# Kernel tuning notes

Hardware: AMD Instinct MI355X
Metric: run time of the kernel (lower is better)

Reference implementation:

```python
import jax, jax.numpy as jnp
import numpy as np

NUM_HEADS = 16


def rotate_half(x):
    half = x.shape[-1] // 2
    return jnp.concatenate((-x[..., half:], x[..., :half]), axis=-1)


def rope_tables(seq_len, head_dim, dtype=jnp.float32):
    inv_freq = 1.0 / (10000.0 ** (jnp.arange(0, head_dim, 2, dtype=jnp.float32) / head_dim))
    t = jnp.arange(seq_len, dtype=jnp.float32)
    freqs = jnp.outer(t, inv_freq)                 # [S, hd/2]
    emb = jnp.concatenate((freqs, freqs), axis=-1)  # [S, hd]
    return jnp.cos(emb).astype(dtype), jnp.sin(emb).astype(dtype)


def setup_inputs() -> dict:
    key = jax.random.key(0)
    k1, k2, k3 = jax.random.split(key, 3)
    B, S, D = 2, 2048, 1024
    x = jax.random.normal(k1, (B, S, D), dtype=jnp.float32)
    # causal lower-triangular mask, broadcast over batch/heads
    mask = jnp.tril(jnp.ones((S, S), dtype=bool))[None, None, :, :]
    w_qkv = jax.random.normal(k2, (3 * D, D), dtype=jnp.float32) * (D ** -0.5)
    w_out = jax.random.normal(k3, (D, D), dtype=jnp.float32) * (D ** -0.5)
    return {"x": x, "mask": mask, "w_qkv": w_qkv, "w_out": w_out}


def reference(x, mask, w_qkv, w_out):
    B, S, D = x.shape
    H = NUM_HEADS
    hd = D // H
    scale = hd ** -0.5

    qkv = jnp.einsum('bsd,ed->bse', x, w_qkv)          # [B, S, 3D]
    q, k, v = jnp.split(qkv, 3, axis=-1)

    def split(t):
        return t.reshape(B, S, H, hd).transpose(0, 2, 1, 3)  # [B, H, S, hd]

    q, k, v = split(q), split(k), split(v)

    cos, sin = rope_tables(S, hd, x.dtype)             # [S, hd]
    cos = cos[None, None]
    sin = sin[None, None]
    q = q * cos + rotate_half(q) * sin
    k = k * cos + rotate_half(k) * sin

    attn = jnp.einsum('bhqd,bhkd->bhqk', q, k) * scale  # [B, H, S, S]
    attn = jnp.where(mask, attn, jnp.float32(-jnp.inf).astype(attn.dtype))
    attn = jax.nn.softmax(attn, axis=-1)
    out = jnp.einsum('bhqk,bhkd->bhqd', attn, v)        # [B, H, S, hd]
    out = out.transpose(0, 2, 1, 3).reshape(B, S, D)
    return jnp.einsum('bsd,ed->bse', out, w_out)
```

## Files before the change

kernel.cpp:

```cpp
#include <hip/hip_runtime.h>
#include <hip/hip_bf16.h>

typedef __attribute__((ext_vector_type(8))) __bf16 bf16x8;
typedef __attribute__((ext_vector_type(4))) __bf16 bf16x4;
typedef __attribute__((ext_vector_type(2))) __bf16 bf16x2;
typedef __attribute__((ext_vector_type(4))) float f32x4;
typedef __attribute__((ext_vector_type(16))) float f32x16;

#define SEQ 2048
#define NH 16
#define HD 64
#define DMODEL 1024
#define BATCH 2
#define MTOT 4096
#define NSLOT 72

#if __has_builtin(__builtin_amdgcn_exp2f)
#define EXP2(x) __builtin_amdgcn_exp2f(x)
#else
#define EXP2(x) exp2f(x)
#endif
#define MFMA32(a, b, c) __builtin_amdgcn_mfma_f32_32x32x16_bf16(a, b, c, 0, 0, 0)

__device__ __forceinline__ void gl_lds16(const void* g, void* l) {
    __builtin_amdgcn_global_load_lds(
        (const __attribute__((address_space(1))) void*)(uintptr_t)g,
        (__attribute__((address_space(3))) void*)(uintptr_t)l,
        16, 0, 0);
}

__device__ __forceinline__ unsigned pk2(float x, float y) {
    union { bf16x2 h; unsigned u; } c;
    c.h = bf16x2{ (__bf16)x, (__bf16)y };
    return c.u;
}

#define TILE_SYNC(N) do {                                           \
    asm volatile("s_waitcnt vmcnt(" #N ")" ::: "memory");           \
    __builtin_amdgcn_s_barrier();                                   \
    __builtin_amdgcn_sched_barrier(0);                              \
} while (0)

__constant__ int4 FITEM[80] = {
    {31,0,16,68},{31,16,32,69},{31,32,48,70},{31,48,64,71},
    {23,0,16,37},{23,16,32,38},{23,32,48,39},
    {15,0,16,14},{15,16,32,15},
    {30,15,31,65},{30,46,62,67},
    {22,30,46,36},
    {7,0,16,-1},
    {29,0,15,60},{29,15,30,61},{29,30,45,62},{29,45,60,63},
    {30,0,15,64},{30,31,46,66},
    {22,0,15,34},{22,15,30,35},
    {21,14,29,32},{21,29,44,33},
    {28,14,29,57},{28,43,58,59},
    {14,0,15,12},{14,15,30,13},
    {27,0,14,52},{27,14,28,53},{27,28,42,54},{27,42,56,55},
    {28,0,14,56},{28,29,43,58},
    {20,0,14,28},{20,14,28,29},{20,28,42,30},
    {21,0,14,31},
    {26,13,27,49},{26,40,54,51},
    {19,26,40,27},
    {13,0,14,10},{13,14,28,11},
    {6,0,14,-1},
    {25,0,13,44},{25,13,26,45},{25,26,39,46},{25,39,52,47},
    {26,0,13,48},{26,27,40,50},
    {24,12,25,41},{24,37,50,43},
    {19,0,13,25},{19,13,26,26},
    {18,12,25,23},{18,25,38,24},
    {12,0,13,8},{12,13,26,9},
    {24,0,12,40},{24,25,37,42},
    {17,0,12,19},{17,12,24,20},{17,24,36,21},
    {18,0,12,22},
    {16,22,34,18},
    {11,0,12,6},{11,12,24,7},
    {5,0,12,-1},
    {16,0,11,16},{16,11,22,17},
    {10,0,11,4},{10,11,22,5},
    {9,0,10,2},{9,10,20,3},
    {4,0,10,-1},
    {8,0,9,0},{8,9,18,1},
    {3,0,8,-1},{2,0,6,-1},{1,0,4,-1},{0,0,2,-1}
};

__global__ __launch_bounds__(256) void cast3(const float4* __restrict__ x,
                                             const float4* __restrict__ wq,
                                             const float4* __restrict__ wo,
                                             __bf16* __restrict__ xb,
                                             __bf16* __restrict__ wqb,
                                             __bf16* __restrict__ wob) {
    const int NX  = 1024 * 1024;
    const int NWQ = 768 * 1024;
    const int NTOT = NX + NWQ + 256 * 1024;
    int i = blockIdx.x * 256 + threadIdx.x;
    if (i >= NTOT) return;
    float4 v; __bf16* dst; int j;
    if (i < NX)            { j = i;            v = x[j];  dst = xb;  }
    else if (i < NX + NWQ) { j = i - NX;       v = wq[j]; dst = wqb; }
    else                   { j = i - NX - NWQ; v = wo[j]; dst = wob; }
    bf16x4 o = { (__bf16)v.x, (__bf16)v.y, (__bf16)v.z, (__bf16)v.w };
    *(bf16x4*)(dst + (size_t)j * 4) = o;
}

__global__ __launch_bounds__(512, 2) void gemm_qkv(const __bf16* __restrict__ A,
                                                   const __bf16* __restrict__ Bt,
                                                   __bf16* __restrict__ Qp,
                                                   char* __restrict__ K2,
                                                   char* __restrict__ V2) {
    const int K = 1024;
    __shared__ __align__(16) char lds[3 * 49152];
    const int tid = threadIdx.x, lane = tid & 63, wave = tid >> 6;
    const int lrow = lane & 15, quad = lane >> 4;
    const int bx = blockIdx.x, by = blockIdx.y;
    const int m0 = by * 256, n0 = bx * 128;
    const int wm = wave >> 1, wn = wave & 1;

    const __bf16* ap[4]; int aof[4];
    const __bf16* bp[2]; int bof[2];
#pragma unroll
    for (int i = 0; i < 4; ++i) {
        int r0 = i * 64 + wave * 8;
        int row = r0 + (lane >> 3);
        int cg = (lane & 7) ^ (row & 7);
        ap[i] = A + (size_t)(m0 + row) * K + cg * 8;
        aof[i] = r0 * 128;
    }
#pragma unroll
    for (int i = 0; i < 2; ++i) {
        int r0 = i * 64 + wave * 8;
        int row = r0 + (lane >> 3);
        int cg = (lane & 7) ^ (row & 7);
        bp[i] = Bt + (size_t)(n0 + row) * K + cg * 8;
        bof[i] = 32768 + r0 * 128;
    }
    int arow[4], brow[4];
#pragma unroll
    for (int i = 0; i < 4; ++i) {
        arow[i] = wm * 64 + i * 16 + lrow;
        brow[i] = wn * 64 + i * 16 + lrow;
    }

    f32x4 z = {0.f, 0.f, 0.f, 0.f};
    f32x4 acc[4][4];
#pragma unroll
    for (int i = 0; i < 4; ++i)
#pragma unroll
        for (int j = 0; j < 4; ++j) acc[i][j] = z;

    auto STAGE = [&](char* base, int k0) {
#pragma unroll
        for (int i = 0; i < 4; ++i) gl_lds16(ap[i] + k0, base + aof[i]);
#pragma unroll
        for (int i = 0; i < 2; ++i) gl_lds16(bp[i] + k0, base + bof[i]);
    };
    auto COMPUTE = [&](const char* base) {
        const char* bb = base + 32768;
#pragma unroll
        for (int ks = 0; ks < 2; ++ks) {
            bf16x8 af[4], bfr[4];
#pragma unroll
            for (int i = 0; i < 4; ++i)
                af[i] = *(const bf16x8*)(base + arow[i] * 128 +
                                         (((ks * 4 + quad) ^ (arow[i] & 7)) << 4));
#pragma unroll
            for (int i = 0; i < 4; ++i)
                bfr[i] = *(const bf16x8*)(bb + brow[i] * 128 +
                                          (((ks * 4 + quad) ^ (brow[i] & 7)) << 4));
            __builtin_amdgcn_s_setprio(1);
#pragma unroll
            for (int i = 0; i < 4; ++i)
#pragma unroll
                for (int j = 0; j < 4; ++j)
                    acc[i][j] = __builtin_amdgcn_mfma_f32_16x16x32_bf16(
                        af[i], bfr[j], acc[i][j], 0, 0, 0);
            __builtin_amdgcn_s_setprio(0);
        }
    };

    STAGE(lds, 0);
    STAGE(lds + 49152, 64);
    TILE_SYNC(6);
    for (int t = 0; t < 14; ++t) {
        STAGE(lds + ((t + 2) % 3) * 49152, (t + 2) * 64);
        COMPUTE(lds + (t % 3) * 49152);
        TILE_SYNC(6);
    }
    COMPUTE(lds + 2 * 49152);
    TILE_SYNC(0);
    COMPUTE(lds);

    const int nt = bx;
    const int sec = nt >> 3;
    const int b = m0 >> 11;
    const int s0b = m0 & (SEQ - 1);
    const int h = (nt & 7) * 2 + wn;
    const int bh = b * NH + h;

    if (sec < 2) {
        const float scale = sec ? 1.0f : 0.18033688011112042f;
        char* Kb = K2 + (size_t)bh * 262144;
        float invf0 = 0.15915494309189535f *
                      exp2f(-(float)lrow * 0.4152410118609203f);
        float invf1 = invf0 * 0.01f;
#pragma unroll
        for (int i = 0; i < 4; ++i) {
            int srow0 = s0b + wm * 64 + i * 16 + quad * 4;
#pragma unroll
            for (int j = 0; j < 2; ++j) {
                float invf = j ? invf1 : invf0;
                int hdlo = j * 16 + lrow;
#pragma unroll
                for (int r = 0; r < 4; ++r) {
                    int s = srow0 + r;
                    float rev = (float)s * invf;
                    float fr = rev - floorf(rev);
                    float sn = __builtin_amdgcn_sinf(fr);
                    float cs = __builtin_amdgcn_cosf(fr);
                    float lo = acc[i][j][r], hi = acc[i][j + 2][r];
                    float olo = (lo * cs - hi * sn) * scale;
                    float ohi = (hi * cs + lo * sn) * scale;
                    if (sec == 0) {
                        size_t base = ((size_t)bh * SEQ + s) * HD + hdlo;
                        Qp[base] = (__bf16)olo;
                        Qp[base + 32] = (__bf16)ohi;
                    } else {
                        char* kt = Kb + (s >> 5) * 4096 + (s & 31) * 16 +
                                   ((lrow >> 3) & 1) * 512 + (lrow & 7) * 2;
                        *(__bf16*)(kt + j * 1024) = (__bf16)olo;
                        *(__bf16*)(kt + (j + 2) * 1024) = (__bf16)ohi;
                    }
                }
            }
        }
    } else {
        char* Vb = V2 + (size_t)bh * 262144;
#pragma unroll
        for (int i = 0; i < 4; ++i) {
            int srow0 = s0b + wm * 64 + i * 16 + quad * 4;
            int kb = srow0 >> 4, ko = srow0 & 15;
            int slot0 = ((ko >> 2) & 1) * 8 + (ko >> 3) * 4;
#pragma unroll
            for (int j = 0; j < 4; ++j) {
                int ch = j * 16 + lrow;
                bf16x4 wv = { (__bf16)acc[i][j][0], (__bf16)acc[i][j][1],
                              (__bf16)acc[i][j][2], (__bf16)acc[i][j][3] };
                *(bf16x4*)(Vb + kb * 2048 + ch * 32 + slot0 * 2) = wv;
            }
        }
    }
}

__global__ __launch_bounds__(256) void gemm_bt(const __bf16* __restrict__ A,
                                               const __bf16* __restrict__ Bt,
                                               float* __restrict__ Cf,
                                               int M, int N, int K) {
    __shared__ __bf16 sA[2][128 * 64];
    __shared__ __bf16 sB[2][128 * 64];
    const int tid = threadIdx.x, lane = tid & 63, wave = tid >> 6;
    const int lrow = lane & 15, quad = lane >> 4;

    int lin = blockIdx.y * 8 + blockIdx.x;
    lin = (lin & 7) * 32 + (lin >> 3);
    const int bx = lin & 7, by = lin >> 3;
    const int m0 = by * 128, n0 = bx * 128;
    const int wm = wave >> 1, wn = wave & 1;

    const __bf16* ap[4]; const __bf16* bp[4]; int ldso[4];
#pragma unroll
    for (int i = 0; i < 4; ++i) {
        int r0 = i * 32 + wave * 8;
        int row = r0 + (lane >> 3);
        int cg = (lane & 7) ^ (row & 7);
        ap[i] = A + (size_t)(m0 + row) * K + cg * 8;
        bp[i] = Bt + (size_t)(n0 + row) * K + cg * 8;
        ldso[i] = r0 * 128;
    }
    int arow[4], brow[4];
#pragma unroll
    for (int i = 0; i < 4; ++i) {
        arow[i] = wm * 64 + i * 16 + lrow;
        brow[i] = wn * 64 + i * 16 + lrow;
    }

    f32x4 z = {0.f, 0.f, 0.f, 0.f};
    f32x4 acc[4][4];
#pragma unroll
    for (int i = 0; i < 4; ++i)
#pragma unroll
        for (int j = 0; j < 4; ++j) acc[i][j] = z;

    char* sA0 = (char*)sA[0]; char* sA1 = (char*)sA[1];
    char* sB0 = (char*)sB[0]; char* sB1 = (char*)sB[1];

    auto STAGE = [&](char* dA, char* dB, int k0) {
#pragma unroll
        for (int i = 0; i < 4; ++i) gl_lds16(ap[i] + k0, dA + ldso[i]);
#pragma unroll
        for (int i = 0; i < 4; ++i) gl_lds16(bp[i] + k0, dB + ldso[i]);
    };
    auto COMPUTE = [&](const char* sAb, const char* sBb) {
#pragma unroll
        for (int ks = 0; ks < 2; ++ks) {
            bf16x8 af[4], bfr[4];
#pragma unroll
            for (int i = 0; i < 4; ++i)
                af[i] = *(const bf16x8*)(sAb + arow[i] * 128 +
                                         (((ks * 4 + quad) ^ (arow[i] & 7)) << 4));
#pragma unroll
            for (int i = 0; i < 4; ++i)
                bfr[i] = *(const bf16x8*)(sBb + brow[i] * 128 +
                                          (((ks * 4 + quad) ^ (brow[i] & 7)) << 4));
#pragma unroll
            for (int i = 0; i < 4; ++i)
#pragma unroll
                for (int j = 0; j < 4; ++j)
                    acc[i][j] = __builtin_amdgcn_mfma_f32_16x16x32_bf16(
                        af[i], bfr[j], acc[i][j], 0, 0, 0);
        }
    };

    STAGE(sA0, sB0, 0);
    __syncthreads();
    for (int k0 = 0; k0 < K; k0 += 128) {
        if (k0 + 64 < K) STAGE(sA1, sB1, k0 + 64);
        COMPUTE(sA0, sB0);
        __syncthreads();
        if (k0 + 128 < K) STAGE(sA0, sB0, k0 + 128);
        COMPUTE(sA1, sB1);
        __syncthreads();
    }
#pragma unroll
    for (int i = 0; i < 4; ++i)
#pragma unroll
        for (int j = 0; j < 4; ++j)
#pragma unroll
            for (int r = 0; r < 4; ++r) {
                int row = m0 + wm * 64 + i * 16 + quad * 4 + r;
                int col = n0 + wn * 64 + j * 16 + lrow;
                Cf[(size_t)row * N + col] = acc[i][j][r];
            }
}

__global__ __launch_bounds__(64) void flash_attn(const __bf16* __restrict__ Qp,
                                                 const char* __restrict__ K2,
                                                 const char* __restrict__ V2,
                                                 __bf16* __restrict__ Aout,
                                                 __bf16* __restrict__ Opart,
                                                 float* __restrict__ Lpart) {
    const int lane = threadIdx.x;
    const int ql = lane & 31, half = lane >> 5;
    const int lin = blockIdx.x;
    const int xcd = lin & 7;
    const int j = lin >> 3;
    const int item = j % 80;
    const int bgroup = j / 80;
    const int bh = bgroup * 8 + xcd;
    const int4 it = FITEM[item];
    const int s = it.x, t0 = it.y, t1 = it.z, slot = it.w;
    const int b = bh >> 4, hh = bh & 15;

    const __bf16* qb = Qp + ((size_t)bh * SEQ + s * 64 + ql) * HD + half * 8;
    bf16x8 qf0[4], qf1[4];
#pragma unroll
    for (int kc = 0; kc < 4; ++kc) {
        qf0[kc] = *(const bf16x8*)(qb + kc * 16);
        qf1[kc] = *(const bf16x8*)(qb + 32 * HD + kc * 16);
    }
    const char* Kb = K2 + (size_t)bh * 262144 + half * 512 + ql * 16;
    const char* Vb = V2 + (size_t)bh * 262144 + ql * 32 + half * 16;

    f32x16 zz = {0.f};
    f32x16 oA0 = zz, oA1 = zz, oB0 = zz, oB1 = zz;
    float lA = 0.f, lB = 0.f;
    const int dA = 2 * s, dB = 2 * s + 1;
    const int thr = ql - 4 * half;

    auto STEP = [&](int t, const bf16x8* kf, bf16x8* kn) {
        bf16x8 vf[2][2];
#pragma unroll
        for (int lo = 0; lo < 2; ++lo) {
            const char* vp = Vb + (t * 2 + lo) * 2048;
            vf[lo][0] = *(const bf16x8*)(vp);
            vf[lo][1] = *(const bf16x8*)(vp + 1024);
        }
        if (t + 1 < t1) {
            const char* kt = Kb + (t + 1) * 4096;
#pragma unroll
            for (int kc = 0; kc < 4; ++kc)
                kn[kc] = *(const bf16x8*)(kt + kc * 1024);
        }
        const bool do0 = (t != dB);
        f32x16 st0 = zz, st1 = zz;
        if (do0) {
#pragma unroll
            for (int kc = 0; kc < 4; ++kc)
                st0 = MFMA32(kf[kc], qf0[kc], st0);
        }
#pragma unroll
        for (int kc = 0; kc < 4; ++kc)
            st1 = MFMA32(kf[kc], qf1[kc], st1);

        if (do0) {
#pragma unroll
            for (int i = 0; i < 16; ++i) st0[i] = EXP2(st0[i]);
            if (t == dA) {
#pragma unroll
                for (int g = 0; g < 4; ++g)
#pragma unroll
                    for (int tt = 0; tt < 4; ++tt)
                        if (8 * g + tt > thr) st0[g * 4 + tt] = 0.f;
            }
#pragma unroll
            for (int i = 0; i < 16; ++i) lA += st0[i];
        }
#pragma unroll
        for (int i = 0; i < 16; ++i) st1[i] = EXP2(st1[i]);
        if (t == dB) {
#pragma unroll
            for (int g = 0; g < 4; ++g)
#pragma unroll
                for (int tt = 0; tt < 4; ++tt)
                    if (8 * g + tt > thr) st1[g * 4 + tt] = 0.f;
        }
#pragma unroll
        for (int i = 0; i < 16; ++i) lB += st1[i];

#pragma unroll
        for (int lo = 0; lo < 2; ++lo) {
            if (do0) {
                union { unsigned u[4]; bf16x8 v; } p0;
#pragma unroll
                for (int d = 0; d < 4; ++d)
                    p0.u[d] = pk2(st0[lo * 8 + 2 * d], st0[lo * 8 + 2 * d + 1]);
                oA0 = MFMA32(vf[lo][0], p0.v, oA0);
                oA1 = MFMA32(vf[lo][1], p0.v, oA1);
            }
            union { unsigned u[4]; bf16x8 v; } p1;
#pragma unroll
            for (int d = 0; d < 4; ++d)
                p1.u[d] = pk2(st1[lo * 8 + 2 * d], st1[lo * 8 + 2 * d + 1]);
            oB0 = MFMA32(vf[lo][0], p1.v, oB0);
            oB1 = MFMA32(vf[lo][1], p1.v, oB1);
        }
    };

    bf16x8 kA[4], kB[4];
    {
        const char* kt = Kb + t0 * 4096;
#pragma unroll
        for (int kc = 0; kc < 4; ++kc)
            kA[kc] = *(const bf16x8*)(kt + kc * 1024);
    }
    int t = t0;
    while (true) {
        STEP(t, kA, kB);
        if (++t >= t1) break;
        STEP(t, kB, kA);
        if (++t >= t1) break;
    }

    lA += __shfl_xor(lA, 32, 64);
    lB += __shfl_xor(lB, 32, 64);

    if (slot < 0) {
        float iA = 1.0f / lA, iB = 1.0f / lB;
        __bf16* oa = Aout + ((size_t)b * SEQ + s * 64 + ql) * DMODEL + hh * HD;
        __bf16* ob = oa + (size_t)32 * DMODEL;
#pragma unroll
        for (int g = 0; g < 4; ++g) {
            bf16x4 wA0 = { (__bf16)(oA0[g*4+0]*iA), (__bf16)(oA0[g*4+1]*iA),
                           (__bf16)(oA0[g*4+2]*iA), (__bf16)(oA0[g*4+3]*iA) };
            bf16x4 wA1 = { (__bf16)(oA1[g*4+0]*iA), (__bf16)(oA1[g*4+1]*iA),
                           (__bf16)(oA1[g*4+2]*iA), (__bf16)(oA1[g*4+3]*iA) };
            bf16x4 wB0 = { (__bf16)(oB0[g*4+0]*iB), (__bf16)(oB0[g*4+1]*iB),
                           (__bf16)(oB0[g*4+2]*iB), (__bf16)(oB0[g*4+3]*iB) };
            bf16x4 wB1 = { (__bf16)(oB1[g*4+0]*iB), (__bf16)(oB1[g*4+1]*iB),
                           (__bf16)(oB1[g*4+2]*iB), (__bf16)(oB1[g*4+3]*iB) };
            *(bf16x4*)(oa + 8 * g + 4 * half) = wA0;
            *(bf16x4*)(oa + 32 + 8 * g + 4 * half) = wA1;
            *(bf16x4*)(ob + 8 * g + 4 * half) = wB0;
            *(bf16x4*)(ob + 32 + 8 * g + 4 * half) = wB1;
        }
    } else {
        __bf16* oa = Opart + ((size_t)(bh * NSLOT + slot) << 12) + ql * 64;
        __bf16* ob = oa + 32 * 64;
#pragma unroll
        for (int g = 0; g < 4; ++g) {
            bf16x4 wA0 = { (__bf16)oA0[g*4+0], (__bf16)oA0[g*4+1],
                           (__bf16)oA0[g*4+2], (__bf16)oA0[g*4+3] };
            bf16x4 wA1 = { (__bf16)oA1[g*4+0], (__bf16)oA1[g*4+1],
                           (__bf16)oA1[g*4+2], (__bf16)oA1[g*4+3] };
            bf16x4 wB0 = { (__bf16)oB0[g*4+0], (__bf16)oB0[g*4+1],
                           (__bf16)oB0[g*4+2], (__bf16)oB0[g*4+3] };
            bf16x4 wB1 = { (__bf16)oB1[g*4+0], (__bf16)oB1[g*4+1],
                           (__bf16)oB1[g*4+2], (__bf16)oB1[g*4+3] };
            *(bf16x4*)(oa + 8 * g + 4 * half) = wA0;
            *(bf16x4*)(oa + 32 + 8 * g + 4 * half) = wA1;
            *(bf16x4*)(ob + 8 * g + 4 * half) = wB0;
            *(bf16x4*)(ob + 32 + 8 * g + 4 * half) = wB1;
        }
        if (!half) {
            Lpart[(bh * NSLOT + slot) * 64 + ql] = lA;
            Lpart[(bh * NSLOT + slot) * 64 + 32 + ql] = lB;
        }
    }
}

__global__ __launch_bounds__(256) void combine(const __bf16* __restrict__ Opart,
                                               const float* __restrict__ Lpart,
                                               __bf16* __restrict__ Aout) {
    const int bh = blockIdx.x;
    const int s = 8 + blockIdx.y;
    const int C = (s < 16) ? 2 : ((s < 24) ? 3 : 4);
    const int base = (s < 16) ? (s - 8) * 2
                   : (s < 24) ? 16 + (s - 16) * 3
                              : 40 + (s - 24) * 4;
    const int t = threadIdx.x;
    const int r = t >> 2, cg = (t & 3) * 16;
    float acc[16];
#pragma unroll
    for (int i = 0; i < 16; ++i) acc[i] = 0.f;
    float l = 0.f;
    for (int ci = 0; ci < C; ++ci) {
        int ch = bh * NSLOT + base + ci;
        l += Lpart[ch * 64 + r];
        const __bf16* p = Opart + ((size_t)ch << 12) + r * 64 + cg;
#pragma unroll
        for (int k = 0; k < 2; ++k) {
            bf16x8 v = ((const bf16x8*)p)[k];
#pragma unroll
            for (int j = 0; j < 8; ++j) acc[k * 8 + j] += (float)v[j];
        }
    }
    float invl = 1.0f / l;
    const int b = bh >> 4, hh = bh & 15;
    __bf16* dst = Aout + ((size_t)(b * SEQ + s * 64 + r)) * DMODEL +
                  hh * 64 + cg;
#pragma unroll
    for (int k = 0; k < 2; ++k) {
        bf16x8 w;
#pragma unroll
        for (int j = 0; j < 8; ++j) w[j] = (__bf16)(acc[k * 8 + j] * invl);
        ((bf16x8*)dst)[k] = w;
    }
}

extern "C" void kernel_launch(void* const* d_in, const int* in_sizes, int n_in,
                              void* d_out, int out_size, void* d_ws, size_t ws_size,
                              hipStream_t stream) {
    (void)in_sizes; (void)n_in; (void)out_size; (void)ws_size;
    const float* x  = (const float*)d_in[0];
    const float* wq = (const float*)d_in[2];
    const float* wo = (const float*)d_in[3];
    float* out = (float*)d_out;

    char* w = (char*)d_ws;
    __bf16* xb   = (__bf16*)(w);
    __bf16* wqb  = (__bf16*)(w + (8ull << 20));
    __bf16* wob  = (__bf16*)(w + (14ull << 20));
    __bf16* Opart= (__bf16*)(w + (16ull << 20));
    float*  Lpart= (float*) (w + (35ull << 20));
    __bf16* Qb   = (__bf16*)(w + (40ull << 20));
    char*   K2   = (char*)  (w + (48ull << 20));
    char*   V2   = (char*)  (w + (56ull << 20));
    __bf16* aob  = xb;

    cast3<<<8192, 256, 0, stream>>>((const float4*)x, (const float4*)wq,
                                    (const float4*)wo, xb, wqb, wob);
    gemm_qkv<<<dim3(24, 16), 512, 0, stream>>>(xb, wqb, Qb, K2, V2);
    flash_attn<<<2560, 64, 0, stream>>>(Qb, K2, V2, aob, Opart, Lpart);
    combine<<<dim3(32, 24), 256, 0, stream>>>(Opart, Lpart, aob);
    gemm_bt<<<dim3(8, 32), 256, 0, stream>>>(aob, wob, out, MTOT, 1024, 1024);
}
```

Before: 184.6 us.

## Prefetch V tiles one step ahead and raise wave priority around MFMA blocks

V fragments for the next key tile are now loaded together with the next K fragments into double-buffered registers, so their global-load latency overlaps the current step's compute instead of stalling the PV MFMAs. The MFMA sections are also wrapped in s_setprio to favour waves issuing matrix work. This costs extra VGPRs for the second V buffer, which may lower occupancy.

```diff
diff --git a/kernel.cpp b/kernel.cpp
--- a/kernel.cpp
+++ b/kernel.cpp
@@ -374,15 +374,14 @@
     const int dA = 2 * s, dB = 2 * s + 1;
     const int thr = ql - 4 * half;
 
-    auto STEP = [&](int t, const bf16x8* kf, bf16x8* kn) {
-        bf16x8 vf[2][2];
-#pragma unroll
-        for (int lo = 0; lo < 2; ++lo) {
-            const char* vp = Vb + (t * 2 + lo) * 2048;
-            vf[lo][0] = *(const bf16x8*)(vp);
-            vf[lo][1] = *(const bf16x8*)(vp + 1024);
-        }
+    auto STEP = [&](int t, const bf16x8* kf, bf16x8* kn,
+                    const bf16x8 (*vf)[2], bf16x8 (*vn)[2]) {
         if (t + 1 < t1) {
+            const char* vp = Vb + ((t + 1) * 2) * 2048;
+            vn[0][0] = *(const bf16x8*)(vp);
+            vn[0][1] = *(const bf16x8*)(vp + 1024);
+            vn[1][0] = *(const bf16x8*)(vp + 2048);
+            vn[1][1] = *(const bf16x8*)(vp + 3072);
             const char* kt = Kb + (t + 1) * 4096;
 #pragma unroll
             for (int kc = 0; kc < 4; ++kc)
@@ -390,6 +389,7 @@
         }
         const bool do0 = (t != dB);
         f32x16 st0 = zz, st1 = zz;
+        __builtin_amdgcn_s_setprio(1);
         if (do0) {
 #pragma unroll
             for (int kc = 0; kc < 4; ++kc)
@@ -398,6 +398,7 @@
 #pragma unroll
         for (int kc = 0; kc < 4; ++kc)
             st1 = MFMA32(kf[kc], qf1[kc], st1);
+        __builtin_amdgcn_s_setprio(0);
 
         if (do0) {
 #pragma unroll
@@ -424,6 +425,7 @@
 #pragma unroll
         for (int i = 0; i < 16; ++i) lB += st1[i];
 
+        __builtin_amdgcn_s_setprio(1);
 #pragma unroll
         for (int lo = 0; lo < 2; ++lo) {
             if (do0) {
@@ -441,20 +443,26 @@
             oB0 = MFMA32(vf[lo][0], p1.v, oB0);
             oB1 = MFMA32(vf[lo][1], p1.v, oB1);
         }
+        __builtin_amdgcn_s_setprio(0);
     };
 
-    bf16x8 kA[4], kB[4];
+    bf16x8 kA[4], kB[4], vA[2][2], vB[2][2];
     {
         const char* kt = Kb + t0 * 4096;
 #pragma unroll
         for (int kc = 0; kc < 4; ++kc)
             kA[kc] = *(const bf16x8*)(kt + kc * 1024);
+        const char* vp = Vb + (t0 * 2) * 2048;
+        vA[0][0] = *(const bf16x8*)(vp);
+        vA[0][1] = *(const bf16x8*)(vp + 1024);
+        vA[1][0] = *(const bf16x8*)(vp + 2048);
+        vA[1][1] = *(const bf16x8*)(vp + 3072);
     }
     int t = t0;
     while (true) {
-        STEP(t, kA, kB);
+        STEP(t, kA, kB, vA, vB);
         if (++t >= t1) break;
-        STEP(t, kB, kA);
+        STEP(t, kB, kA, vB, vA);
         if (++t >= t1) break;
     }
 
```

After: 188.5 us. 2.1% more time.

## Group four attention work items per block and share K/V tiles through LDS

Applied to the files above, without the earlier changes.

Work items are reordered into groups of four with overlapping key ranges. Each 256-thread block now runs one group, one item per wave, and cooperatively stages each K/V tile into a triple-buffered LDS ring with async global-to-LDS loads. Waves skip compute on tiles outside their own range. This cuts redundant global/L2 reads of K/V across items. The cost is block-wide barriers, idle waves when ranges differ, and LDS traffic replacing direct register loads.

```diff
diff --git a/kernel.cpp b/kernel.cpp
--- a/kernel.cpp
+++ b/kernel.cpp
@@ -42,43 +42,25 @@
 } while (0)
 
 __constant__ int4 FITEM[80] = {
-    {31,0,16,68},{31,16,32,69},{31,32,48,70},{31,48,64,71},
-    {23,0,16,37},{23,16,32,38},{23,32,48,39},
-    {15,0,16,14},{15,16,32,15},
-    {30,15,31,65},{30,46,62,67},
-    {22,30,46,36},
-    {7,0,16,-1},
-    {29,0,15,60},{29,15,30,61},{29,30,45,62},{29,45,60,63},
-    {30,0,15,64},{30,31,46,66},
-    {22,0,15,34},{22,15,30,35},
-    {21,14,29,32},{21,29,44,33},
-    {28,14,29,57},{28,43,58,59},
-    {14,0,15,12},{14,15,30,13},
-    {27,0,14,52},{27,14,28,53},{27,28,42,54},{27,42,56,55},
-    {28,0,14,56},{28,29,43,58},
-    {20,0,14,28},{20,14,28,29},{20,28,42,30},
-    {21,0,14,31},
-    {26,13,27,49},{26,40,54,51},
-    {19,26,40,27},
-    {13,0,14,10},{13,14,28,11},
-    {6,0,14,-1},
-    {25,0,13,44},{25,13,26,45},{25,26,39,46},{25,39,52,47},
-    {26,0,13,48},{26,27,40,50},
-    {24,12,25,41},{24,37,50,43},
-    {19,0,13,25},{19,13,26,26},
-    {18,12,25,23},{18,25,38,24},
-    {12,0,13,8},{12,13,26,9},
-    {24,0,12,40},{24,25,37,42},
-    {17,0,12,19},{17,12,24,20},{17,24,36,21},
-    {18,0,12,22},
-    {16,22,34,18},
-    {11,0,12,6},{11,12,24,7},
-    {5,0,12,-1},
-    {16,0,11,16},{16,11,22,17},
-    {10,0,11,4},{10,11,22,5},
-    {9,0,10,2},{9,10,20,3},
-    {4,0,10,-1},
-    {8,0,9,0},{8,9,18,1},
+    {31,0,16,68},{23,0,16,37},{15,0,16,14},{7,0,16,-1},
+    {31,16,32,69},{23,16,32,38},{15,16,32,15},{30,15,31,65},
+    {31,32,48,70},{23,32,48,39},{30,31,46,66},{29,30,45,62},
+    {31,48,64,71},{30,46,62,67},{29,45,60,63},{28,43,58,59},
+    {22,30,46,36},{18,25,38,24},{17,24,36,21},{16,22,34,18},
+    {30,0,15,64},{29,0,15,60},{22,0,15,34},{14,0,15,12},
+    {29,15,30,61},{22,15,30,35},{14,15,30,13},{28,14,29,57},
+    {27,14,28,53},{20,14,28,29},{13,14,28,11},{21,14,29,32},
+    {27,28,42,54},{20,28,42,30},{28,29,43,58},{21,29,44,33},
+    {28,0,14,56},{27,0,14,52},{21,0,14,31},{20,0,14,28},
+    {13,0,14,10},{6,0,14,-1},{25,0,13,44},{26,0,13,48},
+    {26,13,27,49},{25,13,26,45},{19,13,26,26},{12,13,26,9},
+    {26,27,40,50},{25,26,39,46},{19,26,40,27},{24,25,37,42},
+    {26,40,54,51},{25,39,52,47},{24,37,50,43},{27,42,56,55},
+    {19,0,13,25},{12,0,13,8},{5,0,12,-1},{18,0,12,22},
+    {24,12,25,41},{18,12,25,23},{17,12,24,20},{11,12,24,7},
+    {24,0,12,40},{17,0,12,19},{11,0,12,6},{16,0,11,16},
+    {16,11,22,17},{10,11,22,5},{9,10,20,3},{8,9,18,1},
+    {10,0,11,4},{9,0,10,2},{8,0,9,0},{4,0,10,-1},
     {3,0,8,-1},{2,0,6,-1},{1,0,4,-1},{0,0,2,-1}
 };
 
@@ -340,23 +322,29 @@
             }
 }
 
-__global__ __launch_bounds__(64) void flash_attn(const __bf16* __restrict__ Qp,
-                                                 const char* __restrict__ K2,
-                                                 const char* __restrict__ V2,
-                                                 __bf16* __restrict__ Aout,
-                                                 __bf16* __restrict__ Opart,
-                                                 float* __restrict__ Lpart) {
-    const int lane = threadIdx.x;
+__global__ __launch_bounds__(256) void flash_attn(const __bf16* __restrict__ Qp,
+                                                  const char* __restrict__ K2,
+                                                  const char* __restrict__ V2,
+                                                  __bf16* __restrict__ Aout,
+                                                  __bf16* __restrict__ Opart,
+                                                  float* __restrict__ Lpart) {
+    __shared__ __align__(16) char klds[3][8192];
+    const int lane = threadIdx.x & 63;
+    const int wave = threadIdx.x >> 6;
     const int ql = lane & 31, half = lane >> 5;
     const int lin = blockIdx.x;
     const int xcd = lin & 7;
-    const int j = lin >> 3;
-    const int item = j % 80;
-    const int bgroup = j / 80;
+    const int jj = lin >> 3;
+    const int group = jj % 20;
+    const int bgroup = jj / 20;
     const int bh = bgroup * 8 + xcd;
-    const int4 it = FITEM[item];
+    const int4 it = FITEM[group * 4 + wave];
     const int s = it.x, t0 = it.y, t1 = it.z, slot = it.w;
     const int b = bh >> 4, hh = bh & 15;
+    const int4 ga = FITEM[group * 4 + 0], gb = FITEM[group * 4 + 1];
+    const int4 gc = FITEM[group * 4 + 2], gd = FITEM[group * 4 + 3];
+    const int T0 = min(min(ga.y, gb.y), min(gc.y, gd.y));
+    const int T1 = max(max(ga.z, gb.z), max(gc.z, gd.z));
 
     const __bf16* qb = Qp + ((size_t)bh * SEQ + s * 64 + ql) * HD + half * 8;
     bf16x8 qf0[4], qf1[4];
@@ -365,8 +353,8 @@
         qf0[kc] = *(const bf16x8*)(qb + kc * 16);
         qf1[kc] = *(const bf16x8*)(qb + 32 * HD + kc * 16);
     }
-    const char* Kb = K2 + (size_t)bh * 262144 + half * 512 + ql * 16;
-    const char* Vb = V2 + (size_t)bh * 262144 + ql * 32 + half * 16;
+    const char* KbB = K2 + (size_t)bh * 262144;
+    const char* VbB = V2 + (size_t)bh * 262144;
 
     f32x16 zz = {0.f};
     f32x16 oA0 = zz, oA1 = zz, oB0 = zz, oB1 = zz;
@@ -374,19 +362,24 @@
     const int dA = 2 * s, dB = 2 * s + 1;
     const int thr = ql - 4 * half;
 
-    auto STEP = [&](int t, const bf16x8* kf, bf16x8* kn) {
-        bf16x8 vf[2][2];
+    auto STAGET = [&](int bt) {
+        char* dst = klds[bt % 3] + wave * 1024;
+        const char* kg = KbB + (size_t)bt * 4096 + wave * 1024 + lane * 16;
+        const char* vg = VbB + (size_t)bt * 4096 + wave * 1024 + lane * 16;
+        gl_lds16(kg, dst);
+        gl_lds16(vg, dst + 4096);
+    };
+
+    auto STEP = [&](int t, const char* base) {
+        bf16x8 kf[4], vf[2][2];
+#pragma unroll
+        for (int kc = 0; kc < 4; ++kc)
+            kf[kc] = *(const bf16x8*)(base + kc * 1024 + half * 512 + ql * 16);
 #pragma unroll
         for (int lo = 0; lo < 2; ++lo) {
-            const char* vp = Vb + (t * 2 + lo) * 2048;
+            const char* vp = base + 4096 + lo * 2048 + ql * 32 + half * 16;
             vf[lo][0] = *(const bf16x8*)(vp);
             vf[lo][1] = *(const bf16x8*)(vp + 1024);
-        }
-        if (t + 1 < t1) {
-            const char* kt = Kb + (t + 1) * 4096;
-#pragma unroll
-            for (int kc = 0; kc < 4; ++kc)
-                kn[kc] = *(const bf16x8*)(kt + kc * 1024);
         }
         const bool do0 = (t != dB);
         f32x16 st0 = zz, st1 = zz;
@@ -443,19 +436,18 @@
         }
     };
 
-    bf16x8 kA[4], kB[4];
-    {
-        const char* kt = Kb + t0 * 4096;
-#pragma unroll
-        for (int kc = 0; kc < 4; ++kc)
-            kA[kc] = *(const bf16x8*)(kt + kc * 1024);
-    }
-    int t = t0;
-    while (true) {
-        STEP(t, kA, kB);
-        if (++t >= t1) break;
-        STEP(t, kB, kA);
-        if (++t >= t1) break;
+    STAGET(T0);
+    STAGET(T0 + 1);
+    TILE_SYNC(2);
+    for (int bt = T0; bt < T1; ++bt) {
+        if (bt + 2 < T1) {
+            STAGET(bt + 2);
+            if (bt >= t0 && bt < t1) STEP(bt, klds[bt % 3]);
+            TILE_SYNC(2);
+        } else {
+            if (bt >= t0 && bt < t1) STEP(bt, klds[bt % 3]);
+            TILE_SYNC(0);
+        }
     }
 
     lA += __shfl_xor(lA, 32, 64);
@@ -567,7 +559,7 @@
     cast3<<<8192, 256, 0, stream>>>((const float4*)x, (const float4*)wq,
                                     (const float4*)wo, xb, wqb, wob);
     gemm_qkv<<<dim3(24, 16), 512, 0, stream>>>(xb, wqb, Qb, K2, V2);
-    flash_attn<<<2560, 64, 0, stream>>>(Qb, K2, V2, aob, Opart, Lpart);
+    flash_attn<<<640, 256, 0, stream>>>(Qb, K2, V2, aob, Opart, Lpart);
     combine<<<dim3(32, 24), 256, 0, stream>>>(Opart, Lpart, aob);
     gemm_bt<<<dim3(8, 32), 256, 0, stream>>>(aob, wob, out, MTOT, 1024, 1024);
 }
```

Result: slower. 219.3 us (+18.8%).
